# Optimization experiments

Hardware: AMD Instinct MI355X
Metric: run time of the kernel (lower is better)

The kernel has to match this reference:

```python
import jax, jax.numpy as jnp
import numpy as np
from jax import lax

B, T, N, D = 4, 12, 1024, 128
C_FRONT = 78           # front/back channel split used by the mixup
X_LAST = T // 2 - 1    # static row index of the last (only effective) mixup call
BS_ST = 6              # block_size of mixup_region_ST
SIGMA = 10.0
LN_EPS = 1e-5


def _mixup_region_ST(graph, y):
    """Faithful jax port of mixup_region_ST(graph_front, x=X_LAST, y, 6, sigma=10).
    graph: [T, N, C_FRONT] float; y: traced int scalar."""
    T_, N_, C_ = graph.shape
    x = X_LAST  # static python int
    y_start = jnp.maximum(y - BS_ST, 0)
    y_end = jnp.minimum(y + 2 * BS_ST, N_)

    # temporal gaussian mix of column y over rows [0, x), written at (x, y)
    xs = jnp.arange(x, dtype=graph.dtype)
    w = jnp.exp(-((xs - (x - 1.0)) ** 2) / (2.0 * SIGMA ** 2))
    w = w / w.sum()
    target = graph[:x, y, :]                      # [x, C]
    mixed_value = (w[:, None] * target).sum(0)    # [C]
    g = lax.dynamic_update_slice(graph, mixed_value[None, None, :], (x, y, 0))

    def mix_write(g_, bs, maxj):
        # average blocks g_[:, j*bs:(j+1)*bs, :] for j in [y_start//bs, y_end//bs)
        j0 = y_start // bs
        j1 = y_end // bs
        jj = jnp.arange(maxj)
        mask = (jj < (j1 - j0)).astype(g_.dtype)              # [maxj]
        cols = jnp.clip((j0 + jj)[:, None] * bs + jnp.arange(bs)[None, :], 0, N_ - 1)
        blocks = g_[:, cols, :]                               # [T, maxj, bs, C]
        mixed = (blocks * mask[None, :, None, None]).sum(1) / (j1 - j0).astype(g_.dtype)
        # torch writes mixed_region.to(torch.uint8) into a float tensor
        mixed = lax.stop_gradient(mixed.astype(jnp.uint8).astype(g_.dtype))
        return lax.dynamic_update_slice(g_, mixed, (0, y, 0))

    # torch resets block_size to 1 when y_end > w - block_size
    return lax.cond(y_end > N_ - BS_ST,
                    lambda g_: mix_write(g_, 1, 3 * BS_ST),
                    lambda g_: mix_write(g_, BS_ST, 4),
                    g)


def _forward(inp, adapt_G, xff_w, xff_b, ff1_w, ff1_b, ff2_w, ff2_b, ln_w, ln_b):
    x_ = inp @ xff_w.T + xff_b                       # [B,T,N,3D]
    q, k, v = jnp.split(x_, 3, axis=-1)
    e = jnp.einsum('btnd,btmd->btnm', q, k) / (D ** 0.5)
    e = e @ adapt_G                                  # [B,T,N,N]
    attn = jax.nn.softmax(e, axis=-1)
    attn_det = lax.stop_gradient(attn)               # self.attention_maps = attn.detach()

    def process(attn_b, val_b):                      # [T,N,N], [T,N,D]
        front = val_b[..., :C_FRONT]
        back = val_b[..., C_FRONT:]
        col_sums = attn_b.sum(axis=1)                # [T, N]
        _, idx = lax.top_k(-col_sums, 2)             # 2 smallest per row, ascending
        # only the last loop iteration's mixup survives in the original code
        y = idx[X_LAST, 1]
        return jnp.concatenate([_mixup_region_ST(front, y), back], axis=-1)

    new_value = jax.vmap(process)(attn_det, v)       # [B,T,N,D]
    vi = attn @ new_value                            # [B,T,N,D]
    h = jax.nn.gelu(vi @ ff1_w.T + ff1_b, approximate=False)
    h = h @ ff2_w.T + ff2_b
    out = h + inp
    mu = out.mean(-1, keepdims=True)
    var = ((out - mu) ** 2).mean(-1, keepdims=True)
    return (out - mu) / jnp.sqrt(var + LN_EPS) * ln_w + ln_b


def setup_inputs() -> dict:
    key = jax.random.key(0)
    ks = jax.random.split(key, 6)
    s = 0.02
    return {
        'input': jax.random.normal(ks[0], (B, T, N, D), jnp.float32),
        'adapt_G': jax.random.normal(ks[1], (N, N), jnp.float32) / np.float32(np.sqrt(N)),
        'xff_w': jax.random.normal(ks[2], (3 * D, D), jnp.float32) * s,
        'xff_b': jnp.zeros((3 * D,), jnp.float32),
        'ff1_w': jax.random.normal(ks[3], (D, D), jnp.float32) * s,
        'ff1_b': jnp.zeros((D,), jnp.float32),
        'ff2_w': jax.random.normal(ks[4], (D, D), jnp.float32) * s,
        'ff2_b': jnp.zeros((D,), jnp.float32),
        'ln_w': jnp.ones((D,), jnp.float32),
        'ln_b': jnp.zeros((D,), jnp.float32),
    }


def reference(input, adapt_G, xff_w, xff_b, ff1_w, ff1_b, ff2_w, ff2_b, ln_w, ln_b):
    return _forward(input, adapt_G, xff_w, xff_b, ff1_w, ff1_b, ff2_w, ff2_b, ln_w, ln_b)
```

## Files before the change

kernel.cpp:

```cpp
#include <hip/hip_runtime.h>
#include <hip/hip_bf16.h>

typedef __attribute__((ext_vector_type(8))) short bf16x8;
typedef __attribute__((ext_vector_type(4))) float f32x4;
typedef unsigned long long ull;

#define MFMA(a,b,c) __builtin_amdgcn_mfma_f32_16x16x32_bf16((a),(b),(c),0,0,0)
#define VMCNT(N) asm volatile("s_waitcnt vmcnt(%0)" :: "i"(N) : "memory")

__device__ __forceinline__ short f2bs(float f){
  union { float f; unsigned u; } x; x.f = f;
  unsigned r = (x.u + 0x7fffu + ((x.u >> 16) & 1u)) >> 16;
  return (short)r;
}
__device__ __forceinline__ float bs2f(short s){
  union { unsigned u; float f; } x; x.u = ((unsigned)(unsigned short)s) << 16;
  return x.f;
}

__device__ __forceinline__ void gl2lds16(const void* g, void* l){
  __builtin_amdgcn_global_load_lds((const __attribute__((address_space(1))) void*)g,
                                   (__attribute__((address_space(3))) void*)l, 16, 0, 0);
}

__device__ __forceinline__ void merge2(ull& a1, ull& a2, ull b1, ull b2){
  ull n1 = min(a1, b1);
  ull n2 = min(max(a1, b1), min(a2, b2));
  a1 = n1; a2 = n2;
}

__global__ __launch_bounds__(256) void prep_kernel(const float* __restrict__ xffw,
                                                   const float* __restrict__ w1,
                                                   const float* __restrict__ w2,
                                                   const float* __restrict__ G,
                                                   short* __restrict__ wqkv_b,
                                                   short* __restrict__ w1_b,
                                                   short* __restrict__ w2_b,
                                                   short* __restrict__ gt){
  __shared__ float tile[32][33];
  int blk = blockIdx.x;
  if (blk >= 1024){
    int i = (blk-1024)*256 + threadIdx.x;
    int stride = 32*256;
    for (int idx = i; idx < 384*128; idx += stride) wqkv_b[idx] = f2bs(xffw[idx]);
    for (int idx = i; idx < 128*128; idx += stride) w1_b[idx] = f2bs(w1[idx]);
    for (int idx = i; idx < 128*128; idx += stride) w2_b[idx] = f2bs(w2[idx]);
    return;
  }
  int bx = blk & 31;
  int by = blk >> 5;
  int tx = threadIdx.x & 31, ty = threadIdx.x >> 5;
  #pragma unroll
  for (int j=0;j<4;j++){
    int n = by*32 + ty + j*8;
    tile[ty+j*8][tx] = G[(size_t)n*1024 + bx*32 + tx];
  }
  __syncthreads();
  #pragma unroll
  for (int j=0;j<4;j++){
    int m = bx*32 + ty + j*8;
    gt[(size_t)m*1024 + by*32 + tx] = f2bs(tile[tx][ty+j*8]);
  }
}

__global__ __launch_bounds__(256,3) void qkv_kernel(const float* __restrict__ inp,
                                                  const short* __restrict__ wqkv,
                                                  const float* __restrict__ bias,
                                                  short* __restrict__ q, short* __restrict__ kT,
                                                  short* __restrict__ nvt){
  __shared__ __align__(16) char smem[49152];
  int w = threadIdx.x >> 6, lane = threadIdx.x & 63;
  int lr = lane & 15, lg = lane >> 4;
  int r0 = blockIdx.x*64;
  int bt = blockIdx.x >> 4;
  int n0 = r0 & 1023;
  int rw = r0 + w*16;
  bf16x8 a[4];
  #pragma unroll
  for (int kc=0;kc<4;kc++){
    const float* ar = inp + (size_t)(rw+lr)*128 + kc*32 + lg*8;
    float4 f0 = *(const float4*)ar;
    float4 f1 = *(const float4*)(ar+4);
    bf16x8 t;
    t[0]=f2bs(f0.x); t[1]=f2bs(f0.y); t[2]=f2bs(f0.z); t[3]=f2bs(f0.w);
    t[4]=f2bs(f1.x); t[5]=f2bs(f1.y); t[6]=f2bs(f1.z); t[7]=f2bs(f1.w);
    a[kc]=t;
  }
  auto stageW = [&](int buf, int kc){
    #pragma unroll
    for (int t=0;t<6;t++){
      int r = (w*6+t)*16 + (lane>>2);
      int s = (lane&3) ^ ((r>>1)&3);
      gl2lds16(wqkv + (size_t)r*128 + kc*32 + s*8,
               smem + buf*24576 + (w*6+t)*1024);
    }
  };
  f32x4 acc[24];
  #pragma unroll
  for (int j=0;j<24;j++) acc[j] = f32x4{0.f,0.f,0.f,0.f};
  stageW(0, 0);
  int cur = 0;
  for (int kc=0; kc<4; kc++){
    if (kc < 3) { stageW(cur^1, kc+1); VMCNT(6); } else { VMCNT(0); }
    __builtin_amdgcn_s_barrier();
    __builtin_amdgcn_sched_barrier(0);
    const char* wb = smem + cur*24576;
    __builtin_amdgcn_s_setprio(1);
    #pragma unroll
    for (int jt=0;jt<24;jt++){
      int j = jt*16 + lr;
      bf16x8 b = *(const bf16x8*)(wb + (size_t)j*64 + ((lg ^ ((lr>>1)&3))*16));
      acc[jt] = MFMA(a[kc], b, acc[jt]);
    }
    __builtin_amdgcn_s_setprio(0);
    __builtin_amdgcn_s_barrier();
    cur ^= 1;
  }
  #pragma unroll
  for (int jt=0;jt<8;jt++){
    float bj = bias[jt*16+lr];
    #pragma unroll
    for (int rr=0;rr<4;rr++)
      q[(size_t)(rw + lg*4 + rr)*128 + jt*16 + lr] = f2bs(acc[jt][rr] + bj);
  }
  __syncthreads();
  short (*tb)[72] = (short(*)[72])smem;
  #pragma unroll
  for (int jt=8;jt<16;jt++){
    int d = (jt-8)*16 + lr;
    float bj = bias[jt*16+lr];
    #pragma unroll
    for (int rr=0;rr<4;rr++) tb[d][w*16 + lg*4 + rr] = f2bs(acc[jt][rr] + bj);
  }
  __syncthreads();
  #pragma unroll
  for (int it=0;it<4;it++){
    int idx = it*256 + threadIdx.x;
    int row = idx >> 3, c8 = (idx & 7)*8;
    *(bf16x8*)(kT + ((size_t)bt*128 + row)*1024 + n0 + c8) = *(const bf16x8*)&tb[row][c8];
  }
  __syncthreads();
  #pragma unroll
  for (int jt=16;jt<24;jt++){
    int c = (jt-16)*16 + lr;
    float bj = bias[jt*16+lr];
    #pragma unroll
    for (int rr=0;rr<4;rr++) tb[c][w*16 + lg*4 + rr] = f2bs(acc[jt][rr] + bj);
  }
  __syncthreads();
  #pragma unroll
  for (int it=0;it<4;it++){
    int idx = it*256 + threadIdx.x;
    int row = idx >> 3, c8 = (idx & 7)*8;
    *(bf16x8*)(nvt + ((size_t)bt*128 + row)*1024 + n0 + c8) = *(const bf16x8*)&tb[row][c8];
  }
}

__global__ __launch_bounds__(256,3) void kg_kernel(const short* __restrict__ gt,
                                                   const short* __restrict__ kT,
                                                   short* __restrict__ kgt){
  __shared__ __align__(16) short gtl[2][64*64];
  __shared__ __align__(16) short ktl[2][128*64];
  int lb = (blockIdx.x & 7)*96 + (blockIdx.x >> 3);
  int bt = lb >> 4;
  int mt = lb & 15;
  int w = threadIdx.x>>6, lane = threadIdx.x&63, lr = lane&15, lg = lane>>4;
  int mblk = mt*64;
  const short* kbase = kT + (size_t)bt*128*1024;
  auto stage = [&](int b, int nc){
    int n0 = nc*64;
    #pragma unroll
    for (int t=0;t<2;t++){
      int row = w*16 + t*8 + (lane>>3);
      int cswz = ((lane&7)*16) ^ ((row&7)<<4);
      gl2lds16(gt + (size_t)(mblk+row)*1024 + n0 + (cswz>>1),
               (char*)gtl[b] + w*2048 + t*1024);
    }
    #pragma unroll
    for (int t=0;t<4;t++){
      int row = w*32 + t*8 + (lane>>3);
      int cswz = ((lane&7)*16) ^ ((row&7)<<4);
      gl2lds16(kbase + (size_t)row*1024 + n0 + (cswz>>1),
               (char*)ktl[b] + w*4096 + t*1024);
    }
  };
  f32x4 acc[8];
  #pragma unroll
  for (int i=0;i<8;i++) acc[i] = f32x4{0.f,0.f,0.f,0.f};
  stage(0, 0);
  int cur = 0;
  for (int nc=0; nc<16; nc++){
    if (nc < 15) { stage(cur^1, nc+1); VMCNT(6); } else { VMCNT(0); }
    __builtin_amdgcn_s_barrier();
    __builtin_amdgcn_sched_barrier(0);
    __builtin_amdgcn_s_setprio(1);
    #pragma unroll
    for (int ks=0;ks<2;ks++){
      int arl = w*16 + lr;
      int acb = ks*64 + lg*16;
      bf16x8 af = *(const bf16x8*)((const char*)gtl[cur] + arl*128 + (acb ^ ((arl&7)<<4)));
      #pragma unroll
      for (int dt=0;dt<8;dt++){
        int brl = dt*16 + lr;
        bf16x8 bf = *(const bf16x8*)((const char*)ktl[cur] + brl*128 + (acb ^ ((brl&7)<<4)));
        acc[dt] = MFMA(af, bf, acc[dt]);
      }
    }
    __builtin_amdgcn_s_setprio(0);
    __builtin_amdgcn_s_barrier();
    cur ^= 1;
  }
  const float SCALE = 0.08838834764831845f;
  int m = mblk + w*16 + lg*4;
  #pragma unroll
  for (int dt=0;dt<8;dt++){
    #pragma unroll
    for (int rr=0;rr<4;rr++){
      kgt[((size_t)(bt*1024 + m + rr))*128 + dt*16 + lr] = f2bs(acc[dt][rr]*SCALE);
    }
  }
}

__global__ __launch_bounds__(256,3) void fused_kernel(const short* __restrict__ q,
                                                      const short* __restrict__ kgt,
                                                      const short* __restrict__ nvt,
                                                      float* __restrict__ zbuf,
                                                      short* __restrict__ pbuf,
                                                      short* __restrict__ vib){
  __shared__ __align__(16) short kgl[64*128];
  __shared__ __align__(16) short nvl[128*64];
  __shared__ __align__(16) char  p_raw[8192];
  int lb = (blockIdx.x & 7)*96 + (blockIdx.x >> 3);
  int bt = lb >> 4;
  int rblk = lb & 15;
  int w = threadIdx.x>>6, lane = threadIdx.x&63, lr = lane&15, lg = lane>>4;
  int r0 = rblk*64 + w*16;
  bool is5 = (bt % 12) == 5;
  int bq = bt / 12;
  const short* qrow = q + ((size_t)(bt*1024 + r0 + lr))*128;
  bf16x8 a[4];
  #pragma unroll
  for (int kc=0;kc<4;kc++) a[kc] = *(const bf16x8*)(qrow + kc*32 + lg*8);
  const short* kgb = kgt + (size_t)bt*1024*128;
  const short* nvb = nvt + (size_t)bt*128*1024;
  char* pw = p_raw + w*2048;
  auto stage_kg = [&](int mc){
    int m0 = mc*64;
    #pragma unroll
    for (int t=0;t<4;t++){
      int row = w*16 + t*4 + (lane>>4);
      int cswz = ((lane&15)*16) ^ ((row&7)<<4);
      gl2lds16(kgb + (size_t)(m0+row)*128 + (cswz>>1),
               (char*)kgl + w*4096 + t*1024);
    }
  };
  auto stage_nv = [&](int mc){
    int m0 = mc*64;
    #pragma unroll
    for (int t=0;t<4;t++){
      int row = w*32 + t*8 + (lane>>3);
      int cswz = ((lane&7)*16) ^ ((row&7)<<4);
      gl2lds16(nvb + (size_t)row*1024 + m0 + (cswz>>1),
               (char*)nvl + w*4096 + t*1024);
    }
  };
  f32x4 acc[8];
  #pragma unroll
  for (int i=0;i<8;i++) acc[i] = f32x4{0.f,0.f,0.f,0.f};
  float zacc[4] = {0.f,0.f,0.f,0.f};
  stage_kg(0);
  stage_nv(0);
  VMCNT(0);
  __builtin_amdgcn_s_barrier();
  __builtin_amdgcn_sched_barrier(0);
  for (int mc=0; mc<16; mc++){
    int m0 = mc*64;
    __builtin_amdgcn_s_setprio(1);
    #pragma unroll
    for (int s=0;s<4;s++){
      f32x4 e = f32x4{0.f,0.f,0.f,0.f};
      #pragma unroll
      for (int kc=0;kc<4;kc++){
        int rl = s*16 + lr;
        int cb = kc*64 + lg*16;
        bf16x8 kb = *(const bf16x8*)((const char*)kgl + rl*256 + (cb ^ ((rl&7)<<4)));
        e = MFMA(a[kc], kb, e);
      }
      #pragma unroll
      for (int rr=0;rr<4;rr++){
        int row = lg*4+rr;
        float p = __expf(fminf(e[rr], 60.f));
        zacc[rr] += p;
        *(short*)(pw + ((row*128 + (s*16+lr)*2) ^ ((row&7)<<4))) = f2bs(p);
      }
    }
    __builtin_amdgcn_s_setprio(0);
    __builtin_amdgcn_s_barrier();
    if (mc < 15) stage_kg(mc+1);
    if (mc < 15) { VMCNT(4); } else { VMCNT(0); }
    __builtin_amdgcn_s_barrier();
    __builtin_amdgcn_sched_barrier(0);
    bf16x8 pa0 = *(const bf16x8*)(pw + ((lr*128 + lg*16) ^ ((lr&7)<<4)));
    bf16x8 pa1 = *(const bf16x8*)(pw + ((lr*128 + 64 + lg*16) ^ ((lr&7)<<4)));
    __builtin_amdgcn_s_setprio(1);
    #pragma unroll
    for (int ct=0; ct<8; ct++){
      int c = ct*16 + lr;
      int mb0 = lg*16;
      int mb1 = 64 + lg*16;
      bf16x8 nb0 = *(const bf16x8*)((const char*)nvl + c*128 + (mb0 ^ ((c&7)<<4)));
      bf16x8 nb1 = *(const bf16x8*)((const char*)nvl + c*128 + (mb1 ^ ((c&7)<<4)));
      acc[ct] = MFMA(pa0, nb0, acc[ct]);
      acc[ct] = MFMA(pa1, nb1, acc[ct]);
    }
    __builtin_amdgcn_s_setprio(0);
    if (is5){
      #pragma unroll
      for (int tt=0; tt<4; tt++){
        int row = tt*4 + (lane>>4);
        int m = (lane&15)*4;
        ull v = *(const ull*)(pw + ((row*128 + m*2) ^ ((row&7)<<4)));
        *(ull*)(pbuf + ((size_t)bq*1024 + r0 + row)*1024 + m0 + m) = v;
      }
    }
    __builtin_amdgcn_s_barrier();
    if (mc < 15) { stage_nv(mc+1); VMCNT(4); } else { VMCNT(0); }
    __builtin_amdgcn_s_barrier();
    __builtin_amdgcn_sched_barrier(0);
  }
  #pragma unroll
  for (int d=1;d<16;d<<=1){
    #pragma unroll
    for (int rr=0;rr<4;rr++) zacc[rr] += __shfl_xor(zacc[rr], d, 64);
  }
  if (lr==0){
    #pragma unroll
    for (int rr=0;rr<4;rr++) zbuf[(size_t)bt*1024 + r0 + lg*4 + rr] = zacc[rr];
  }
  float inv[4];
  #pragma unroll
  for (int rr=0;rr<4;rr++) inv[rr] = 1.0f/zacc[rr];
  #pragma unroll
  for (int ct=0;ct<8;ct++){
    #pragma unroll
    for (int rr=0;rr<4;rr++){
      vib[((size_t)(bt*1024 + r0 + lg*4 + rr))*128 + ct*16 + lr] = f2bs(acc[ct][rr]*inv[rr]);
    }
  }
}

__global__ __launch_bounds__(256) void colsum_kernel(const short* __restrict__ pbuf,
                                                     const float* __restrict__ zbuf,
                                                     float* __restrict__ csfinal){
  __shared__ float part[4][64];
  int b = blockIdx.x >> 4, mg = blockIdx.x & 15;
  int t = threadIdx.x;
  int mcol = mg*64 + (t & 63);
  int rq = t >> 6;
  const short* pb = pbuf + (size_t)b*1024*1024;
  const float* zb = zbuf + (size_t)(b*12 + 5)*1024;
  float s = 0.f;
  for (int r = rq*256; r < rq*256 + 256; r++){
    s += bs2f(pb[(size_t)r*1024 + mcol]) * (1.0f/zb[r]);
  }
  part[rq][t & 63] = s;
  __syncthreads();
  if (t < 64){
    float cs = (part[0][t] + part[1][t]) + (part[2][t] + part[3][t]);
    csfinal[(size_t)b*1024 + mg*64 + t] = cs;
  }
}

__global__ __launch_bounds__(256) void top2_kernel(const float* __restrict__ csfinal,
                                                   int* __restrict__ yidx){
  __shared__ ull s1[4], s2[4];
  int b = blockIdx.x;
  ull b1 = ~0ull, b2 = ~0ull;
  #pragma unroll
  for (int j=0;j<4;j++){
    int col = j*256 + threadIdx.x;
    float s = csfinal[(size_t)b*1024 + col];
    union { float f; unsigned u; } cv; cv.f = s;
    ull key = ((ull)cv.u << 32) | (unsigned)col;
    merge2(b1, b2, key, ~0ull);
  }
  #pragma unroll
  for (int d=1;d<64;d<<=1){
    ull o1 = __shfl_xor(b1, d, 64);
    ull o2 = __shfl_xor(b2, d, 64);
    merge2(b1, b2, o1, o2);
  }
  int w = threadIdx.x >> 6;
  if ((threadIdx.x & 63) == 0){ s1[w] = b1; s2[w] = b2; }
  __syncthreads();
  if (threadIdx.x == 0){
    ull r1 = s1[0], r2 = s2[0];
    merge2(r1, r2, s1[1], s2[1]);
    merge2(r1, r2, s1[2], s2[2]);
    merge2(r1, r2, s1[3], s2[3]);
    yidx[b] = (int)(r2 & 0xffffffffu);
  }
}

__global__ void nvfixA_kernel(const short* __restrict__ nvt, const int* __restrict__ yidx,
                              float* __restrict__ mixres){
  int bt = blockIdx.x; int b = bt/12, t = bt%12;
  int y = yidx[b];
  int y_start = max(y-6, 0), y_end = min(y+12, 1024);
  int bs, j0, cnt;
  if (y_end > 1024-6){ bs = 1; j0 = y_start; cnt = y_end - y_start; }
  else { bs = 6; j0 = y_start/6; cnt = y_end/6 - j0; }
  int items = bs*78;
  int idx = threadIdx.x;
  if (idx >= items) return;
  int i = idx / 78, c = idx % 78;
  const short* nvb = nvt + (size_t)bt*128*1024;
  float acc = 0.f;
  for (int jj=0;jj<cnt;jj++){
    int col = (j0+jj)*bs + i;
    float gv;
    if (t == 5 && col == y){
      float wsum = 0.f, mv = 0.f;
      #pragma unroll
      for (int tp=0;tp<5;tp++){
        float d = (float)tp - 4.0f;
        float w = __expf(-d*d/200.0f);
        wsum += w;
        mv += w * bs2f(nvt[((size_t)(b*12+tp)*128 + c)*1024 + y]);
      }
      gv = mv / wsum;
    } else {
      gv = bs2f(nvb[(size_t)c*1024 + col]);
    }
    acc += gv;
  }
  mixres[((size_t)bt*6 + i)*78 + c] = acc / (float)cnt;
}

__global__ __launch_bounds__(256) void corr_kernel(const short* __restrict__ q,
                                                   const short* __restrict__ kgt,
                                                   const short* __restrict__ nvt,
                                                   const float* __restrict__ mixres,
                                                   const float* __restrict__ zbuf,
                                                   const int* __restrict__ yidx,
                                                   short* __restrict__ vib){
  __shared__ __align__(16) short kcol[6][128];
  __shared__ float delta[6][78];
  int bt = blockIdx.x >> 2;
  int rc = blockIdx.x & 3;
  int b = bt/12;
  int y = yidx[b];
  int y_end = min(y+12, 1024);
  int bs = (y_end > 1024-6) ? 1 : 6;
  for (int idx = threadIdx.x; idx < 6*128; idx += 256){
    int i = idx >> 7, d = idx & 127;
    kcol[i][d] = (i < bs) ? kgt[((size_t)(bt*1024 + y + i))*128 + d] : (short)0;
  }
  for (int idx = threadIdx.x; idx < 6*78; idx += 256){
    int i = idx / 78, c = idx % 78;
    float dv = 0.f;
    if (i < bs){
      float avg = mixres[((size_t)bt*6 + i)*78 + c];
      int ti = (int)avg;
      unsigned char u = (unsigned char)ti;
      dv = (float)u - bs2f(nvt[((size_t)bt*128 + c)*1024 + (y+i)]);
    }
    delta[i][c] = dv;
  }
  __syncthreads();
  int r = rc*256 + threadIdx.x;
  const short* qr = q + ((size_t)(bt*1024 + r))*128;
  float e[6] = {0.f,0.f,0.f,0.f,0.f,0.f};
  for (int d0 = 0; d0 < 128; d0 += 8){
    bf16x8 qv = *(const bf16x8*)(qr + d0);
    #pragma unroll
    for (int j=0;j<8;j++){
      float qf = bs2f(qv[j]);
      #pragma unroll
      for (int i=0;i<6;i++) e[i] += qf * bs2f(kcol[i][d0+j]);
    }
  }
  float invz = 1.0f / zbuf[(size_t)bt*1024 + r];
  float p[6];
  #pragma unroll
  for (int i=0;i<6;i++) p[i] = (i < bs) ? __expf(fminf(e[i],60.f))*invz : 0.f;
  short* vr = vib + ((size_t)(bt*1024 + r))*128;
  for (int c=0;c<78;c++){
    float dsum = 0.f;
    #pragma unroll
    for (int i=0;i<6;i++) dsum += p[i]*delta[i][c];
    vr[c] = f2bs(bs2f(vr[c]) + dsum);
  }
}

__global__ __launch_bounds__(256,3) void ffn_kernel(const short* __restrict__ vib,
                                                  const float* __restrict__ inp,
                                                  const short* __restrict__ w1b,
                                                  const short* __restrict__ w2b,
                                                  const float* __restrict__ b1,
                                                  const float* __restrict__ b2,
                                                  const float* __restrict__ lnw,
                                                  const float* __restrict__ lnb,
                                                  float* __restrict__ out){
  __shared__ __align__(16) short wl[128*128];
  __shared__ __align__(16) short h_lds[4][16][136];
  int w = threadIdx.x>>6, lane = threadIdx.x&63, lr = lane&15, lg = lane>>4;
  int r0 = blockIdx.x*64 + w*16;
  auto stageW = [&](const short* src){
    #pragma unroll
    for (int t=0;t<8;t++){
      int r = (w*8+t)*4 + (lane>>4);
      int s = (lane&15) ^ (r&7);
      gl2lds16(src + (size_t)r*128 + s*8, (char*)wl + (w*8+t)*1024);
    }
  };
  stageW(w1b);
  bf16x8 a[4];
  #pragma unroll
  for (int kc=0;kc<4;kc++) a[kc] = *(const bf16x8*)(vib + (size_t)(r0+lr)*128 + kc*32 + lg*8);
  __syncthreads();
  f32x4 acc[8];
  #pragma unroll
  for (int i=0;i<8;i++) acc[i] = f32x4{0.f,0.f,0.f,0.f};
  __builtin_amdgcn_s_setprio(1);
  #pragma unroll
  for (int kc=0;kc<4;kc++){
    #pragma unroll
    for (int jt=0;jt<8;jt++){
      bf16x8 b = *(const bf16x8*)((const char*)wl + (size_t)(jt*16+lr)*256 + (((kc*4+lg) ^ (lr&7))*16));
      acc[jt] = MFMA(a[kc], b, acc[jt]);
    }
  }
  __builtin_amdgcn_s_setprio(0);
  #pragma unroll
  for (int jt=0;jt<8;jt++){
    float bj = b1[jt*16+lr];
    #pragma unroll
    for (int rr=0;rr<4;rr++){
      float x = acc[jt][rr] + bj;
      float g = 0.5f*x*(1.0f + erff(x*0.70710678118654752f));
      h_lds[w][lg*4+rr][jt*16+lr] = f2bs(g);
    }
  }
  __syncthreads();
  stageW(w2b);
  bf16x8 ha[4];
  #pragma unroll
  for (int kc=0;kc<4;kc++) ha[kc] = *(const bf16x8*)&h_lds[w][lr][kc*32 + lg*8];
  __syncthreads();
  f32x4 acc2[8];
  #pragma unroll
  for (int i=0;i<8;i++) acc2[i] = f32x4{0.f,0.f,0.f,0.f};
  __builtin_amdgcn_s_setprio(1);
  #pragma unroll
  for (int kc=0;kc<4;kc++){
    #pragma unroll
    for (int jt=0;jt<8;jt++){
      bf16x8 b = *(const bf16x8*)((const char*)wl + (size_t)(jt*16+lr)*256 + (((kc*4+lg) ^ (lr&7))*16));
      acc2[jt] = MFMA(ha[kc], b, acc2[jt]);
    }
  }
  __builtin_amdgcn_s_setprio(0);
  float xv[8][4];
  #pragma unroll
  for (int jt=0;jt<8;jt++){
    float bj = b2[jt*16+lr];
    #pragma unroll
    for (int rr=0;rr<4;rr++){
      xv[jt][rr] = acc2[jt][rr] + bj + inp[(size_t)(r0 + lg*4 + rr)*128 + jt*16 + lr];
    }
  }
  float mu[4], rstd[4];
  #pragma unroll
  for (int rr=0;rr<4;rr++){
    float s = 0.f;
    #pragma unroll
    for (int jt=0;jt<8;jt++) s += xv[jt][rr];
    #pragma unroll
    for (int m=1;m<16;m<<=1) s += __shfl_xor(s, m, 64);
    mu[rr] = s * (1.0f/128.0f);
  }
  #pragma unroll
  for (int rr=0;rr<4;rr++){
    float s = 0.f;
    #pragma unroll
    for (int jt=0;jt<8;jt++){ float d = xv[jt][rr]-mu[rr]; s += d*d; }
    #pragma unroll
    for (int m=1;m<16;m<<=1) s += __shfl_xor(s, m, 64);
    rstd[rr] = rsqrtf(s * (1.0f/128.0f) + 1e-5f);
  }
  #pragma unroll
  for (int jt=0;jt<8;jt++){
    int col = jt*16 + lr;
    float lw = lnw[col], lb = lnb[col];
    #pragma unroll
    for (int rr=0;rr<4;rr++){
      out[(size_t)(r0 + lg*4 + rr)*128 + col] = (xv[jt][rr]-mu[rr])*rstd[rr]*lw + lb;
    }
  }
}

extern "C" void kernel_launch(void* const* d_in, const int* in_sizes, int n_in,
                              void* d_out, int out_size, void* d_ws, size_t ws_size,
                              hipStream_t stream) {
  (void)in_sizes; (void)n_in; (void)out_size;
  const float* inp  = (const float*)d_in[0];
  const float* G    = (const float*)d_in[1];
  const float* xffw = (const float*)d_in[2];
  const float* xffb = (const float*)d_in[3];
  const float* w1   = (const float*)d_in[4];
  const float* b1   = (const float*)d_in[5];
  const float* w2   = (const float*)d_in[6];
  const float* b2   = (const float*)d_in[7];
  const float* lnw  = (const float*)d_in[8];
  const float* lnb  = (const float*)d_in[9];
  float* out = (float*)d_out;
  char* ws = (char*)d_ws;

  size_t off = 0;
  auto take = [&](size_t bytes)->char*{ char* p = ws + off; off += (bytes + 255) & ~(size_t)255; return p; };
  short* wqkv_b = (short*)take(384*128*2);
  short* gt_b   = (short*)take((size_t)1024*1024*2);
  short* w1_b   = (short*)take(128*128*2);
  short* w2_b   = (short*)take(128*128*2);
  short* qb     = (short*)take((size_t)48*1024*128*2);
  short* kTb    = (short*)take((size_t)48*128*1024*2);
  short* nvt    = (short*)take((size_t)48*128*1024*2);
  short* kgt    = (short*)take((size_t)48*1024*128*2);
  float* zbuf   = (float*)take((size_t)48*1024*4);
  short* pbuf   = (short*)take((size_t)4*1024*1024*2);
  float* csfin  = (float*)take((size_t)4*1024*4);
  int*   yidx   = (int*)take(256);
  float* mixres = (float*)take((size_t)48*6*78*4);
  short* vibuf  = (short*)take((size_t)48*1024*128*2);
  if (off > ws_size) return;

  prep_kernel<<<dim3(1056), dim3(256), 0, stream>>>(xffw, w1, w2, G, wqkv_b, w1_b, w2_b, gt_b);
  qkv_kernel<<<dim3(768), dim3(256), 0, stream>>>(inp, wqkv_b, xffb, qb, kTb, nvt);
  kg_kernel<<<dim3(768), dim3(256), 0, stream>>>(gt_b, kTb, kgt);
  fused_kernel<<<dim3(768), dim3(256), 0, stream>>>(qb, kgt, nvt, zbuf, pbuf, vibuf);
  colsum_kernel<<<dim3(64), dim3(256), 0, stream>>>(pbuf, zbuf, csfin);
  top2_kernel<<<dim3(4), dim3(256), 0, stream>>>(csfin, yidx);
  nvfixA_kernel<<<dim3(48), dim3(512), 0, stream>>>(nvt, yidx, mixres);
  corr_kernel<<<dim3(192), dim3(256), 0, stream>>>(qb, kgt, nvt, mixres, zbuf, yidx, vibuf);
  ffn_kernel<<<dim3(768), dim3(256), 0, stream>>>(vibuf, inp, w1_b, w2_b, b1, b2, lnw, lnb, out);
}
```

Baseline: 151.6 us.

## Fuse mixup correction into FFN kernel and switch softmax to exp2 with padded LDS

Removes the separate correction kernel by folding the low-rank mixup delta update into the FFN kernel's A-operand load, so the vi buffer is no longer read and written an extra time and one launch disappears. The attention scale now includes log2(e) so the fused kernel can use exp2f instead of __expf. The P tile in LDS switches from an XOR swizzle to a row stride padded to 136 bytes. The cost is that every FFN block recomputes the six q·k correction scores for its rows, and the delta values are now stored as bf16.

Measured after the change: 144.3 us. 1.05x faster.

```diff
diff --git a/kernel.cpp b/kernel.cpp
--- a/kernel.cpp
+++ b/kernel.cpp
@@ -210,7 +210,7 @@
     __builtin_amdgcn_s_barrier();
     cur ^= 1;
   }
-  const float SCALE = 0.08838834764831845f;
+  const float SCALE = 0.08838834764831845f * 1.4426950408889634f;
   int m = mblk + w*16 + lg*4;
   #pragma unroll
   for (int dt=0;dt<8;dt++){
@@ -229,7 +229,7 @@
                                                       short* __restrict__ vib){
   __shared__ __align__(16) short kgl[64*128];
   __shared__ __align__(16) short nvl[128*64];
-  __shared__ __align__(16) char  p_raw[8192];
+  __shared__ __align__(16) char  p_raw[4*2176];
   int lb = (blockIdx.x & 7)*96 + (blockIdx.x >> 3);
   int bt = lb >> 4;
   int rblk = lb & 15;
@@ -243,7 +243,7 @@
   for (int kc=0;kc<4;kc++) a[kc] = *(const bf16x8*)(qrow + kc*32 + lg*8);
   const short* kgb = kgt + (size_t)bt*1024*128;
   const short* nvb = nvt + (size_t)bt*128*1024;
-  char* pw = p_raw + w*2048;
+  char* pw = p_raw + w*2176;
   auto stage_kg = [&](int mc){
     int m0 = mc*64;
     #pragma unroll
@@ -289,9 +289,9 @@
       #pragma unroll
       for (int rr=0;rr<4;rr++){
         int row = lg*4+rr;
-        float p = __expf(fminf(e[rr], 60.f));
+        float p = exp2f(fminf(e[rr], 80.f));
         zacc[rr] += p;
-        *(short*)(pw + ((row*128 + (s*16+lr)*2) ^ ((row&7)<<4))) = f2bs(p);
+        *(short*)(pw + row*136 + (s*16+lr)*2) = f2bs(p);
       }
     }
     __builtin_amdgcn_s_setprio(0);
@@ -300,8 +300,12 @@
     if (mc < 15) { VMCNT(4); } else { VMCNT(0); }
     __builtin_amdgcn_s_barrier();
     __builtin_amdgcn_sched_barrier(0);
-    bf16x8 pa0 = *(const bf16x8*)(pw + ((lr*128 + lg*16) ^ ((lr&7)<<4)));
-    bf16x8 pa1 = *(const bf16x8*)(pw + ((lr*128 + 64 + lg*16) ^ ((lr&7)<<4)));
+    const short* prow = (const short*)(pw + lr*136);
+    bf16x8 pa0, pa1;
+    { ull lo = *(const ull*)(prow + lg*8);      ull hi = *(const ull*)(prow + lg*8 + 4);
+      ((ull*)&pa0)[0] = lo; ((ull*)&pa0)[1] = hi; }
+    { ull lo = *(const ull*)(prow + 64 + lg*8); ull hi = *(const ull*)(prow + 64 + lg*8 + 4);
+      ((ull*)&pa1)[0] = lo; ((ull*)&pa1)[1] = hi; }
     __builtin_amdgcn_s_setprio(1);
     #pragma unroll
     for (int ct=0; ct<8; ct++){
@@ -319,7 +323,7 @@
       for (int tt=0; tt<4; tt++){
         int row = tt*4 + (lane>>4);
         int m = (lane&15)*4;
-        ull v = *(const ull*)(pw + ((row*128 + m*2) ^ ((row&7)<<4)));
+        ull v = *(const ull*)(pw + row*136 + m*2);
         *(ull*)(pbuf + ((size_t)bq*1024 + r0 + row)*1024 + m0 + m) = v;
       }
     }
@@ -437,24 +441,37 @@
   mixres[((size_t)bt*6 + i)*78 + c] = acc / (float)cnt;
 }
 
-__global__ __launch_bounds__(256) void corr_kernel(const short* __restrict__ q,
-                                                   const short* __restrict__ kgt,
-                                                   const short* __restrict__ nvt,
-                                                   const float* __restrict__ mixres,
-                                                   const float* __restrict__ zbuf,
-                                                   const int* __restrict__ yidx,
-                                                   short* __restrict__ vib){
-  __shared__ __align__(16) short kcol[6][128];
-  __shared__ float delta[6][78];
-  int bt = blockIdx.x >> 2;
-  int rc = blockIdx.x & 3;
+__global__ __launch_bounds__(256,3) void ffn_kernel(const short* __restrict__ vib,
+                                                  const float* __restrict__ inp,
+                                                  const short* __restrict__ w1b,
+                                                  const short* __restrict__ w2b,
+                                                  const float* __restrict__ b1,
+                                                  const float* __restrict__ b2,
+                                                  const float* __restrict__ lnw,
+                                                  const float* __restrict__ lnb,
+                                                  const short* __restrict__ qb,
+                                                  const short* __restrict__ kgt,
+                                                  const short* __restrict__ nvt,
+                                                  const float* __restrict__ mixres,
+                                                  const float* __restrict__ zbuf,
+                                                  const int* __restrict__ yidx,
+                                                  float* __restrict__ out){
+  __shared__ __align__(16) short wl[128*128];
+  __shared__ __align__(16) short h_lds[4][16][132];
+  __shared__ __align__(16) short kcol_sh[6*128];
+  __shared__ short delta_sh[6*80];
+  __shared__ float p_sh[64][6];
+  int w = threadIdx.x>>6, lane = threadIdx.x&63, lr = lane&15, lg = lane>>4;
+  int r0 = blockIdx.x*64 + w*16;
+  int r0g = blockIdx.x*64;
+  int bt = blockIdx.x >> 4;
   int b = bt/12;
   int y = yidx[b];
   int y_end = min(y+12, 1024);
   int bs = (y_end > 1024-6) ? 1 : 6;
   for (int idx = threadIdx.x; idx < 6*128; idx += 256){
     int i = idx >> 7, d = idx & 127;
-    kcol[i][d] = (i < bs) ? kgt[((size_t)(bt*1024 + y + i))*128 + d] : (short)0;
+    kcol_sh[idx] = (i < bs) ? kgt[((size_t)(bt*1024 + y + i))*128 + d] : (short)0;
   }
   for (int idx = threadIdx.x; idx < 6*78; idx += 256){
     int i = idx / 78, c = idx % 78;
@@ -465,47 +482,23 @@
       unsigned char u = (unsigned char)ti;
       dv = (float)u - bs2f(nvt[((size_t)bt*128 + c)*1024 + (y+i)]);
     }
-    delta[i][c] = dv;
-  }
-  __syncthreads();
-  int r = rc*256 + threadIdx.x;
-  const short* qr = q + ((size_t)(bt*1024 + r))*128;
-  float e[6] = {0.f,0.f,0.f,0.f,0.f,0.f};
-  for (int d0 = 0; d0 < 128; d0 += 8){
-    bf16x8 qv = *(const bf16x8*)(qr + d0);
-    #pragma unroll
-    for (int j=0;j<8;j++){
-      float qf = bs2f(qv[j]);
+    delta_sh[i*80 + c] = f2bs(dv);
+  }
+  __syncthreads();
+  for (int idx = threadIdx.x; idx < 64*6; idx += 256){
+    int row = idx / 6, i = idx % 6;
+    int R = r0g + row;
+    float e = 0.f;
+    const short* qr = qb + ((size_t)(bt*1024 + R))*128;
+    for (int d0 = 0; d0 < 128; d0 += 8){
+      bf16x8 qv = *(const bf16x8*)(qr + d0);
       #pragma unroll
-      for (int i=0;i<6;i++) e[i] += qf * bs2f(kcol[i][d0+j]);
-    }
-  }
-  float invz = 1.0f / zbuf[(size_t)bt*1024 + r];
-  float p[6];
-  #pragma unroll
-  for (int i=0;i<6;i++) p[i] = (i < bs) ? __expf(fminf(e[i],60.f))*invz : 0.f;
-  short* vr = vib + ((size_t)(bt*1024 + r))*128;
-  for (int c=0;c<78;c++){
-    float dsum = 0.f;
-    #pragma unroll
-    for (int i=0;i<6;i++) dsum += p[i]*delta[i][c];
-    vr[c] = f2bs(bs2f(vr[c]) + dsum);
-  }
-}
-
-__global__ __launch_bounds__(256,3) void ffn_kernel(const short* __restrict__ vib,
-                                                  const float* __restrict__ inp,
-                                                  const short* __restrict__ w1b,
-                                                  const short* __restrict__ w2b,
-                                                  const float* __restrict__ b1,
-                                                  const float* __restrict__ b2,
-                                                  const float* __restrict__ lnw,
-                                                  const float* __restrict__ lnb,
-                                                  float* __restrict__ out){
-  __shared__ __align__(16) short wl[128*128];
-  __shared__ __align__(16) short h_lds[4][16][136];
-  int w = threadIdx.x>>6, lane = threadIdx.x&63, lr = lane&15, lg = lane>>4;
-  int r0 = blockIdx.x*64 + w*16;
+      for (int j=0;j<8;j++) e += bs2f(qv[j]) * bs2f(kcol_sh[i*128 + d0 + j]);
+    }
+    float pv = 0.f;
+    if (i < bs) pv = exp2f(fminf(e, 80.f)) / zbuf[(size_t)bt*1024 + R];
+    p_sh[row][i] = pv;
+  }
   auto stageW = [&](const short* src){
     #pragma unroll
     for (int t=0;t<8;t++){
@@ -515,10 +508,26 @@
     }
   };
   stageW(w1b);
+  __syncthreads();
+  float pr6[6];
+  #pragma unroll
+  for (int i=0;i<6;i++) pr6[i] = p_sh[w*16 + lr][i];
   bf16x8 a[4];
   #pragma unroll
-  for (int kc=0;kc<4;kc++) a[kc] = *(const bf16x8*)(vib + (size_t)(r0+lr)*128 + kc*32 + lg*8);
-  __syncthreads();
+  for (int kc=0;kc<4;kc++){
+    bf16x8 v = *(const bf16x8*)(vib + (size_t)(r0+lr)*128 + kc*32 + lg*8);
+    #pragma unroll
+    for (int e=0;e<8;e++){
+      int col = kc*32 + lg*8 + e;
+      if (col < 78){
+        float ds = 0.f;
+        #pragma unroll
+        for (int i=0;i<6;i++) ds += pr6[i] * bs2f(delta_sh[i*80 + col]);
+        v[e] = f2bs(bs2f(v[e]) + ds);
+      }
+    }
+    a[kc] = v;
+  }
   f32x4 acc[8];
   #pragma unroll
   for (int i=0;i<8;i++) acc[i] = f32x4{0.f,0.f,0.f,0.f};
@@ -527,8 +536,8 @@
   for (int kc=0;kc<4;kc++){
     #pragma unroll
     for (int jt=0;jt<8;jt++){
-      bf16x8 b = *(const bf16x8*)((const char*)wl + (size_t)(jt*16+lr)*256 + (((kc*4+lg) ^ (lr&7))*16));
-      acc[jt] = MFMA(a[kc], b, acc[jt]);
+      bf16x8 bfr = *(const bf16x8*)((const char*)wl + (size_t)(jt*16+lr)*256 + (((kc*4+lg) ^ (lr&7))*16));
+      acc[jt] = MFMA(a[kc], bfr, acc[jt]);
     }
   }
   __builtin_amdgcn_s_setprio(0);
@@ -546,7 +555,12 @@
   stageW(w2b);
   bf16x8 ha[4];
   #pragma unroll
-  for (int kc=0;kc<4;kc++) ha[kc] = *(const bf16x8*)&h_lds[w][lr][kc*32 + lg*8];
+  for (int kc=0;kc<4;kc++){
+    const short* hp = &h_lds[w][lr][kc*32 + lg*8];
+    ull lo = *(const ull*)hp;
+    ull hi = *(const ull*)(hp + 4);
+    ((ull*)&ha[kc])[0] = lo; ((ull*)&ha[kc])[1] = hi;
+  }
   __syncthreads();
   f32x4 acc2[8];
   #pragma unroll
@@ -556,8 +570,8 @@
   for (int kc=0;kc<4;kc++){
     #pragma unroll
     for (int jt=0;jt<8;jt++){
-      bf16x8 b = *(const bf16x8*)((const char*)wl + (size_t)(jt*16+lr)*256 + (((kc*4+lg) ^ (lr&7))*16));
-      acc2[jt] = MFMA(ha[kc], b, acc2[jt]);
+      bf16x8 bfr = *(const bf16x8*)((const char*)wl + (size_t)(jt*16+lr)*256 + (((kc*4+lg) ^ (lr&7))*16));
+      acc2[jt] = MFMA(ha[kc], bfr, acc2[jt]);
     }
   }
   __builtin_amdgcn_s_setprio(0);
@@ -642,6 +656,6 @@
   colsum_kernel<<<dim3(64), dim3(256), 0, stream>>>(pbuf, zbuf, csfin);
   top2_kernel<<<dim3(4), dim3(256), 0, stream>>>(csfin, yidx);
   nvfixA_kernel<<<dim3(48), dim3(512), 0, stream>>>(nvt, yidx, mixres);
-  corr_kernel<<<dim3(192), dim3(256), 0, stream>>>(qb, kgt, nvt, mixres, zbuf, yidx, vibuf);
-  ffn_kernel<<<dim3(768), dim3(256), 0, stream>>>(vibuf, inp, w1_b, w2_b, b1, b2, lnw, lnb, out);
-}
+  ffn_kernel<<<dim3(768), dim3(256), 0, stream>>>(vibuf, inp, w1_b, w2_b, b1, b2, lnw, lnb,
+                                                  qb, kgt, nvt, mixres, zbuf, yidx, out);
+}
```
